# Optimization experiments

Measured on AMD Instinct MI355X. Metric: run time of the kernel, lower is better.

The kernel has to match this reference:

```python
import jax, jax.numpy as jnp
import numpy as np

EPS = 1e-5

def _layernorm(x, g, b):
    mu = jnp.mean(x, axis=-1, keepdims=True)
    var = jnp.var(x, axis=-1, keepdims=True)
    return (x - mu) * jax.lax.rsqrt(var + EPS) * g + b

def setup_inputs() -> dict:
    key = jax.random.key(0)
    ks = jax.random.split(key, 8)
    N, K, E, H = 20000, 32, 256, 128
    return {
        "edge_features": jax.random.normal(ks[0], (N, K, E), dtype=jnp.float32),
        "neighbor_mask": jax.random.randint(ks[1], (N, K), 0, 2) > 0,
        "W_lin": jax.random.normal(ks[2], (E, H), dtype=jnp.float32) / np.sqrt(E),
        "b_lin": jnp.zeros((H,), jnp.float32),
        "g_edge": jnp.ones((H,), jnp.float32),
        "b_edge": jnp.zeros((H,), jnp.float32),
        "W1": jax.random.normal(ks[3], (H, H), dtype=jnp.float32) / np.sqrt(H),
        "b1": jnp.zeros((H,), jnp.float32),
        "W2": jax.random.normal(ks[4], (H, H), dtype=jnp.float32) / np.sqrt(H),
        "b2": jnp.zeros((H,), jnp.float32),
        "g_node": jnp.ones((H,), jnp.float32),
        "b_node": jnp.zeros((H,), jnp.float32),
    }

def reference(edge_features, neighbor_mask, W_lin, b_lin, g_edge, b_edge,
              W1, b1, W2, b2, g_node, b_node):
    # edge_linear: [N,K,E] -> [N,K,H]
    edge_hidden = jnp.einsum('nke,eh->nkh', edge_features, W_lin) + b_lin
    # pre-norm FFN with residual: h + FFN(LN(h))
    h_norm = _layernorm(edge_hidden, g_edge, b_edge)
    ffn = jnp.einsum('nkh,hf->nkf', jax.nn.gelu(jnp.einsum('nkh,hf->nkf', h_norm, W1) + b1), W2) + b2
    edge_output = edge_hidden + ffn
    # masked scatter-aggregate over neighbors -> nodes
    mask = neighbor_mask[..., None].astype(edge_output.dtype)  # [N,K,1]
    node_output = jnp.sum(edge_output * mask, axis=1)  # [N,H]
    # block-level node normalization
    node_output = _layernorm(node_output, g_node, b_node)
    return (node_output, edge_output)
```

## Files before the change

### kernel.cpp

```cpp
#include <hip/hip_runtime.h>

typedef __attribute__((ext_vector_type(8))) short bfrag;
typedef __attribute__((ext_vector_type(4))) float ffrag;

struct alignas(16) U8v { unsigned int u[4]; };

__device__ __forceinline__ unsigned int cvt_pk_bf16(float lo, float hi) {
    unsigned int r;
    asm("v_cvt_pk_bf16_f32 %0, %1, %2" : "=v"(r) : "v"(lo), "v"(hi));
    return r;
}
__device__ __forceinline__ unsigned short f2bf1(float x) {
    return (unsigned short)cvt_pk_bf16(x, x);
}

__global__ void prep_kernel(const float* __restrict__ Wlin,
                            const float* __restrict__ W1,
                            const float* __restrict__ W2,
                            unsigned short* __restrict__ wlinT,
                            unsigned short* __restrict__ w1T,
                            unsigned short* __restrict__ w2T) {
    int idx = blockIdx.x * 256 + threadIdx.x;
    {
        int e = idx >> 7, h = idx & 127;
        wlinT[h * 256 + e] = f2bf1(Wlin[idx]);
    }
    if (idx < 128 * 128) {
        int h = idx >> 7, f = idx & 127;
        w1T[f * 128 + h] = f2bf1(W1[idx]);
        w2T[f * 128 + h] = f2bf1(W2[idx]);
    }
}

__global__ __launch_bounds__(512, 4) void fused_kernel(
    const float* __restrict__ ef, const int* __restrict__ mask,
    const unsigned short* __restrict__ wlinT,
    const unsigned short* __restrict__ w1T,
    const unsigned short* __restrict__ w2T,
    const float* __restrict__ b_lin, const float* __restrict__ g_edge,
    const float* __restrict__ b_edge, const float* __restrict__ b1,
    const float* __restrict__ b2, const float* __restrict__ g_node,
    const float* __restrict__ b_node,
    float* __restrict__ out_node, float* __restrict__ out_edge, int N) {

    __shared__ char  smem[32768];
    __shared__ float s_part[1024];
    __shared__ float s_stat[128];
    __shared__ float s_mask[64];
    __shared__ float s_nv[256];

    const int tid = threadIdx.x;
    const int w = tid >> 6, lane = tid & 63, q = lane >> 4, c = lane & 15;
    const int col = 16 * w + c;

    int row_base = blockIdx.x * 64;
    if (row_base + 64 > N * 32) row_base = N * 32 - 64;
    const int n0 = row_base >> 5;
    const float* efb = ef + (size_t)row_base * 256;

    if (tid < 64) s_mask[tid] = (mask[(size_t)row_base + tid] != 0) ? 1.f : 0.f;

    #pragma unroll
    for (int i = 0; i < 4; ++i) {
        int s = i * 512 + tid;
        int row = s >> 5, cs = s & 31;
        const float4* p = (const float4*)(efb + (size_t)s * 8);
        float4 v0 = p[0], v1 = p[1];
        U8v u;
        u.u[0] = cvt_pk_bf16(v0.x, v0.y); u.u[1] = cvt_pk_bf16(v0.z, v0.w);
        u.u[2] = cvt_pk_bf16(v1.x, v1.y); u.u[3] = cvt_pk_bf16(v1.z, v1.w);
        *(U8v*)(smem + row * 512 + ((cs * 16) ^ ((row & 7) << 4))) = u;
    }
    __syncthreads();

    ffrag acc[4] = {};
    #pragma unroll
    for (int kk = 0; kk < 8; ++kk) {
        bfrag b = *(const bfrag*)(wlinT + col * 256 + kk * 32 + q * 8);
        #pragma unroll
        for (int mt = 0; mt < 4; ++mt) {
            int row = 16 * mt + c;
            bfrag a = *(const bfrag*)(smem + row * 512 + ((kk * 64 + q * 16) ^ ((row & 7) << 4)));
            acc[mt] = __builtin_amdgcn_mfma_f32_16x16x32_bf16(a, b, acc[mt], 0, 0, 0);
        }
    }
    {
        float bl = b_lin[col];
        #pragma unroll
        for (int mt = 0; mt < 4; ++mt)
            #pragma unroll
            for (int r = 0; r < 4; ++r) acc[mt][r] += bl;
    }

    #pragma unroll
    for (int mt = 0; mt < 4; ++mt)
        #pragma unroll
        for (int r = 0; r < 4; ++r) {
            float s = acc[mt][r], qv = acc[mt][r] * acc[mt][r];
            #pragma unroll
            for (int d = 1; d < 16; d <<= 1) { s += __shfl_xor(s, d); qv += __shfl_xor(qv, d); }
            if (c == 0) {
                int row = 16 * mt + 4 * q + r;
                s_part[w * 128 + row * 2]     = s;
                s_part[w * 128 + row * 2 + 1] = qv;
            }
        }
    __syncthreads();
    if (tid < 64) {
        float s = 0.f, qv = 0.f;
        #pragma unroll
        for (int ww = 0; ww < 8; ++ww) { s += s_part[ww * 128 + tid * 2]; qv += s_part[ww * 128 + tid * 2 + 1]; }
        float mu = s * (1.f / 128.f);
        float var = qv * (1.f / 128.f) - mu * mu;
        s_stat[tid] = mu;
        s_stat[64 + tid] = rsqrtf(var + 1e-5f);
    }
    __syncthreads();

    {
        float ge = g_edge[col], be = b_edge[col];
        #pragma unroll
        for (int mt = 0; mt < 4; ++mt)
            #pragma unroll
            for (int r = 0; r < 4; ++r) {
                int row = 16 * mt + 4 * q + r;
                float x = (acc[mt][r] - s_stat[row]) * s_stat[64 + row] * ge + be;
                *(unsigned short*)(smem + row * 256 + ((col * 2) ^ ((row & 7) << 4))) = f2bf1(x);
            }
    }
    __syncthreads();

    ffrag acc2[4] = {};
    #pragma unroll
    for (int kk = 0; kk < 4; ++kk) {
        bfrag b = *(const bfrag*)(w1T + col * 128 + kk * 32 + q * 8);
        #pragma unroll
        for (int mt = 0; mt < 4; ++mt) {
            int row = 16 * mt + c;
            bfrag a = *(const bfrag*)(smem + row * 256 + ((kk * 64 + q * 16) ^ ((row & 7) << 4)));
            acc2[mt] = __builtin_amdgcn_mfma_f32_16x16x32_bf16(a, b, acc2[mt], 0, 0, 0);
        }
    }
    {
        float b1c = b1[col];
        #pragma unroll
        for (int mt = 0; mt < 4; ++mt)
            #pragma unroll
            for (int r = 0; r < 4; ++r) {
                int row = 16 * mt + 4 * q + r;
                float x = acc2[mt][r] + b1c;
                float y = 0.7978845608028654f * x * (1.f + 0.044715f * x * x);
                float e;
                asm("v_exp_f32 %0, %1" : "=v"(e) : "v"(-2.885390081777927f * y));
                float rcp;
                asm("v_rcp_f32 %0, %1" : "=v"(rcp) : "v"(1.f + e));
                float ge = x * rcp;
                *(unsigned short*)(smem + 16384 + row * 256 + ((col * 2) ^ ((row & 7) << 4))) = f2bf1(ge);
            }
    }
    __syncthreads();

    ffrag acc3[4] = {};
    #pragma unroll
    for (int kk = 0; kk < 4; ++kk) {
        bfrag b = *(const bfrag*)(w2T + col * 128 + kk * 32 + q * 8);
        #pragma unroll
        for (int mt = 0; mt < 4; ++mt) {
            int row = 16 * mt + c;
            bfrag a = *(const bfrag*)(smem + 16384 + row * 256 + ((kk * 64 + q * 16) ^ ((row & 7) << 4)));
            acc3[mt] = __builtin_amdgcn_mfma_f32_16x16x32_bf16(a, b, acc3[mt], 0, 0, 0);
        }
    }
    {
        float b2c = b2[col];
        float* eo = out_edge + (size_t)row_base * 128;
        float nvA = 0.f, nvB = 0.f;
        #pragma unroll
        for (int mt = 0; mt < 4; ++mt)
            #pragma unroll
            for (int r = 0; r < 4; ++r) {
                int row = 16 * mt + 4 * q + r;
                float v = acc3[mt][r] + b2c + acc[mt][r];
                eo[row * 128 + col] = v;
                float mv = s_mask[row] * v;
                if (mt < 2) nvA += mv; else nvB += mv;
            }
        nvA += __shfl_xor(nvA, 16); nvA += __shfl_xor(nvA, 32);
        nvB += __shfl_xor(nvB, 16); nvB += __shfl_xor(nvB, 32);
        if (q == 0) { s_nv[col] = nvA; s_nv[128 + col] = nvB; }
    }
    __syncthreads();

    if (w < 2) {
        float v0 = s_nv[w * 128 + lane], v1 = s_nv[w * 128 + 64 + lane];
        float s = v0 + v1, qv = v0 * v0 + v1 * v1;
        #pragma unroll
        for (int d = 1; d < 64; d <<= 1) { s += __shfl_xor(s, d); qv += __shfl_xor(qv, d); }
        float mu = s * (1.f / 128.f);
        float rstd = rsqrtf(qv * (1.f / 128.f) - mu * mu + 1e-5f);
        size_t base = (size_t)(n0 + w) * 128;
        out_node[base + lane]      = (v0 - mu) * rstd * g_node[lane]      + b_node[lane];
        out_node[base + 64 + lane] = (v1 - mu) * rstd * g_node[64 + lane] + b_node[64 + lane];
    }
}

extern "C" void kernel_launch(void* const* d_in, const int* in_sizes, int n_in,
                              void* d_out, int out_size, void* d_ws, size_t ws_size,
                              hipStream_t stream) {
    const float* ef     = (const float*)d_in[0];
    const int*   mask   = (const int*)d_in[1];
    const float* Wlin   = (const float*)d_in[2];
    const float* b_lin  = (const float*)d_in[3];
    const float* g_edge = (const float*)d_in[4];
    const float* b_edge = (const float*)d_in[5];
    const float* W1     = (const float*)d_in[6];
    const float* b1     = (const float*)d_in[7];
    const float* W2     = (const float*)d_in[8];
    const float* b2     = (const float*)d_in[9];
    const float* g_node = (const float*)d_in[10];
    const float* b_node = (const float*)d_in[11];

    int N = in_sizes[0] / (32 * 256);

    unsigned short* wlinT = (unsigned short*)d_ws;
    unsigned short* w1T   = wlinT + 128 * 256;
    unsigned short* w2T   = w1T + 128 * 128;

    float* out_node = (float*)d_out;
    float* out_edge = out_node + (size_t)N * 128;

    prep_kernel<<<128, 256, 0, stream>>>(Wlin, W1, W2, wlinT, w1T, w2T);
    int npairs = (N + 1) / 2;
    fused_kernel<<<npairs, 512, 0, stream>>>(ef, mask, wlinT, w1T, w2T,
                                             b_lin, g_edge, b_edge, b1, b2,
                                             g_node, b_node, out_node, out_edge, N);
}
```

Before: 356.5 us.

## Give each wave its own 16-row tile and fold LayerNorm affine into W1

The kernel now uses 256-thread blocks where each wave owns 16 edge rows across all 128 hidden columns. Edge features are loaded straight from global memory into MFMA fragments, so the shared staging step is gone, and LayerNorm statistics are reduced inside a wave with no block barriers. The edge-norm gain and bias are folded into a pre-scaled W1 and a fused bias by a new prep kernel. Edge outputs are staged through LDS for coalesced float4 stores. The intent is to remove most __syncthreads and LDS traffic, at the cost of more registers (8 accumulator tiles per stage) and weight fragments re-read from global memory per wave.

Result: slower. 715.2 us (+100.6%).

```diff
diff --git a/kernel.cpp b/kernel.cpp
--- a/kernel.cpp
+++ b/kernel.cpp
@@ -3,7 +3,7 @@
 typedef __attribute__((ext_vector_type(8))) short bfrag;
 typedef __attribute__((ext_vector_type(4))) float ffrag;
 
-struct alignas(16) U8v { unsigned int u[4]; };
+union BFU { bfrag f; unsigned int u[4]; };
 
 __device__ __forceinline__ unsigned int cvt_pk_bf16(float lo, float hi) {
     unsigned int r;
@@ -14,193 +14,174 @@
     return (unsigned short)cvt_pk_bf16(x, x);
 }
 
-__global__ void prep_kernel(const float* __restrict__ Wlin,
-                            const float* __restrict__ W1,
-                            const float* __restrict__ W2,
-                            unsigned short* __restrict__ wlinT,
-                            unsigned short* __restrict__ w1T,
-                            unsigned short* __restrict__ w2T) {
+__global__ void prep1(const float* __restrict__ Wlin, const float* __restrict__ W2,
+                      unsigned short* __restrict__ wlinT, unsigned short* __restrict__ w2T) {
     int idx = blockIdx.x * 256 + threadIdx.x;
-    {
-        int e = idx >> 7, h = idx & 127;
-        wlinT[h * 256 + e] = f2bf1(Wlin[idx]);
-    }
-    if (idx < 128 * 128) {
-        int h = idx >> 7, f = idx & 127;
-        w1T[f * 128 + h] = f2bf1(W1[idx]);
-        w2T[f * 128 + h] = f2bf1(W2[idx]);
-    }
-}
-
-__global__ __launch_bounds__(512, 4) void fused_kernel(
+    { int e = idx >> 7, h = idx & 127; wlinT[h * 256 + e] = f2bf1(Wlin[idx]); }
+    if (idx < 16384) { int a = idx >> 7, b = idx & 127; w2T[b * 128 + a] = f2bf1(W2[idx]); }
+}
+
+__global__ void prep2(const float* __restrict__ W1, const float* __restrict__ g_edge,
+                      const float* __restrict__ b_edge, const float* __restrict__ b1,
+                      unsigned short* __restrict__ w1gT, float* __restrict__ b1f) {
+    int f = threadIdx.x;
+    float s = b1[f];
+    for (int h = 0; h < 128; ++h) {
+        float wv = W1[h * 128 + f];
+        w1gT[f * 128 + h] = f2bf1(g_edge[h] * wv);
+        s += b_edge[h] * wv;
+    }
+    b1f[f] = s;
+}
+
+__global__ __launch_bounds__(256, 4) void fused_kernel(
     const float* __restrict__ ef, const int* __restrict__ mask,
     const unsigned short* __restrict__ wlinT,
-    const unsigned short* __restrict__ w1T,
+    const unsigned short* __restrict__ w1gT,
     const unsigned short* __restrict__ w2T,
-    const float* __restrict__ b_lin, const float* __restrict__ g_edge,
-    const float* __restrict__ b_edge, const float* __restrict__ b1,
+    const float* __restrict__ b_lin, const float* __restrict__ b1f,
     const float* __restrict__ b2, const float* __restrict__ g_node,
     const float* __restrict__ b_node,
     float* __restrict__ out_node, float* __restrict__ out_edge, int N) {
 
-    __shared__ char  smem[32768];
-    __shared__ float s_part[1024];
-    __shared__ float s_stat[128];
-    __shared__ float s_mask[64];
-    __shared__ float s_nv[256];
+    __shared__ char lds[4 * 8704];
+    __shared__ float nvlds[4][128];
 
     const int tid = threadIdx.x;
-    const int w = tid >> 6, lane = tid & 63, q = lane >> 4, c = lane & 15;
-    const int col = 16 * w + c;
-
-    int row_base = blockIdx.x * 64;
-    if (row_base + 64 > N * 32) row_base = N * 32 - 64;
-    const int n0 = row_base >> 5;
-    const float* efb = ef + (size_t)row_base * 256;
-
-    if (tid < 64) s_mask[tid] = (mask[(size_t)row_base + tid] != 0) ? 1.f : 0.f;
-
-    #pragma unroll
-    for (int i = 0; i < 4; ++i) {
-        int s = i * 512 + tid;
-        int row = s >> 5, cs = s & 31;
-        const float4* p = (const float4*)(efb + (size_t)s * 8);
-        float4 v0 = p[0], v1 = p[1];
-        U8v u;
-        u.u[0] = cvt_pk_bf16(v0.x, v0.y); u.u[1] = cvt_pk_bf16(v0.z, v0.w);
-        u.u[2] = cvt_pk_bf16(v1.x, v1.y); u.u[3] = cvt_pk_bf16(v1.z, v1.w);
-        *(U8v*)(smem + row * 512 + ((cs * 16) ^ ((row & 7) << 4))) = u;
+    const int w = tid >> 6, l = tid & 63, q = l >> 4, c = l & 15;
+
+    int rb_blk = blockIdx.x * 64;
+    if (rb_blk + 64 > N * 32) rb_blk = N * 32 - 64;
+    const int rb = rb_blk + w * 16;
+
+    char* Z  = lds + w * 8704;
+    char* G  = Z + 4352;
+    char* EO = Z;
+
+    ffrag h8[8] = {};
+    const float* efrow = ef + (size_t)(rb + c) * 256;
+    #pragma unroll 2
+    for (int kk = 0; kk < 8; ++kk) {
+        const float4* bp = (const float4*)(efrow + kk * 32 + 8 * q);
+        float4 e0 = bp[0], e1 = bp[1];
+        BFU bb;
+        bb.u[0] = cvt_pk_bf16(e0.x, e0.y); bb.u[1] = cvt_pk_bf16(e0.z, e0.w);
+        bb.u[2] = cvt_pk_bf16(e1.x, e1.y); bb.u[3] = cvt_pk_bf16(e1.z, e1.w);
+        #pragma unroll
+        for (int t = 0; t < 8; ++t) {
+            bfrag a = *(const bfrag*)(wlinT + (16 * t + c) * 256 + kk * 32 + 8 * q);
+            h8[t] = __builtin_amdgcn_mfma_f32_16x16x32_bf16(a, bb.f, h8[t], 0, 0, 0);
+        }
+    }
+
+    float sum = 0.f, sq = 0.f;
+    #pragma unroll
+    for (int t = 0; t < 8; ++t)
+        #pragma unroll
+        for (int r = 0; r < 4; ++r) {
+            float v = h8[t][r] + b_lin[16 * t + 4 * q + r];
+            h8[t][r] = v;
+            sum += v; sq += v * v;
+        }
+    sum += __shfl_xor(sum, 16); sum += __shfl_xor(sum, 32);
+    sq  += __shfl_xor(sq, 16);  sq  += __shfl_xor(sq, 32);
+    const float mu = sum * (1.f / 128.f);
+    const float rs = rsqrtf(sq * (1.f / 128.f) - mu * mu + 1e-5f);
+
+    #pragma unroll
+    for (int t = 0; t < 8; ++t) {
+        *(unsigned int*)(Z + c * 272 + 32 * t + 8 * q) =
+            cvt_pk_bf16((h8[t][0] - mu) * rs, (h8[t][1] - mu) * rs);
+        *(unsigned int*)(Z + c * 272 + 32 * t + 8 * q + 4) =
+            cvt_pk_bf16((h8[t][2] - mu) * rs, (h8[t][3] - mu) * rs);
+    }
+
+    ffrag acc2[8] = {};
+    #pragma unroll
+    for (int kk = 0; kk < 4; ++kk) {
+        bfrag zb = *(const bfrag*)(Z + c * 272 + kk * 64 + 16 * q);
+        #pragma unroll
+        for (int t = 0; t < 8; ++t) {
+            bfrag a = *(const bfrag*)(w1gT + (16 * t + c) * 128 + kk * 32 + 8 * q);
+            acc2[t] = __builtin_amdgcn_mfma_f32_16x16x32_bf16(a, zb, acc2[t], 0, 0, 0);
+        }
+    }
+
+    #pragma unroll
+    for (int t = 0; t < 8; ++t) {
+        float gg[4];
+        #pragma unroll
+        for (int r = 0; r < 4; ++r) {
+            float x = acc2[t][r] + b1f[16 * t + 4 * q + r];
+            float y = 0.7978845608028654f * x * (1.f + 0.044715f * x * x);
+            float e;
+            asm("v_exp_f32 %0, %1" : "=v"(e) : "v"(-2.885390081777927f * y));
+            float rcp;
+            asm("v_rcp_f32 %0, %1" : "=v"(rcp) : "v"(1.f + e));
+            gg[r] = x * rcp;
+        }
+        *(unsigned int*)(G + c * 272 + 32 * t + 8 * q)     = cvt_pk_bf16(gg[0], gg[1]);
+        *(unsigned int*)(G + c * 272 + 32 * t + 8 * q + 4) = cvt_pk_bf16(gg[2], gg[3]);
+    }
+
+    ffrag acc3[8] = {};
+    #pragma unroll
+    for (int kk = 0; kk < 4; ++kk) {
+        bfrag gb = *(const bfrag*)(G + c * 272 + kk * 64 + 16 * q);
+        #pragma unroll
+        for (int t = 0; t < 8; ++t) {
+            bfrag a = *(const bfrag*)(w2T + (16 * t + c) * 128 + kk * 32 + 8 * q);
+            acc3[t] = __builtin_amdgcn_mfma_f32_16x16x32_bf16(a, gb, acc3[t], 0, 0, 0);
+        }
+    }
+
+    #pragma unroll
+    for (int t = 0; t < 8; ++t)
+        #pragma unroll
+        for (int r = 0; r < 4; ++r) {
+            float v = acc3[t][r] + b2[16 * t + 4 * q + r] + h8[t][r];
+            *(float*)(EO + c * 528 + (16 * t + 4 * q + r) * 4) = v;
+        }
+
+    float4 nva = make_float4(0.f, 0.f, 0.f, 0.f);
+    float4 nvb = make_float4(0.f, 0.f, 0.f, 0.f);
+    float* eob = out_edge + (size_t)rb * 128;
+    #pragma unroll
+    for (int rr = 0; rr < 4; ++rr) {
+        int row = rr * 4 + q;
+        float4 va = *(const float4*)(EO + row * 528 + c * 16);
+        float4 vb = *(const float4*)(EO + row * 528 + 256 + c * 16);
+        *(float4*)(eob + row * 128 + c * 4)      = va;
+        *(float4*)(eob + row * 128 + 64 + c * 4) = vb;
+        float m = (mask[rb + row] != 0) ? 1.f : 0.f;
+        nva.x += m * va.x; nva.y += m * va.y; nva.z += m * va.z; nva.w += m * va.w;
+        nvb.x += m * vb.x; nvb.y += m * vb.y; nvb.z += m * vb.z; nvb.w += m * vb.w;
+    }
+    nva.x += __shfl_xor(nva.x, 16); nva.x += __shfl_xor(nva.x, 32);
+    nva.y += __shfl_xor(nva.y, 16); nva.y += __shfl_xor(nva.y, 32);
+    nva.z += __shfl_xor(nva.z, 16); nva.z += __shfl_xor(nva.z, 32);
+    nva.w += __shfl_xor(nva.w, 16); nva.w += __shfl_xor(nva.w, 32);
+    nvb.x += __shfl_xor(nvb.x, 16); nvb.x += __shfl_xor(nvb.x, 32);
+    nvb.y += __shfl_xor(nvb.y, 16); nvb.y += __shfl_xor(nvb.y, 32);
+    nvb.z += __shfl_xor(nvb.z, 16); nvb.z += __shfl_xor(nvb.z, 32);
+    nvb.w += __shfl_xor(nvb.w, 16); nvb.w += __shfl_xor(nvb.w, 32);
+    if (q == 0) {
+        *(float4*)(&nvlds[w][4 * c])      = nva;
+        *(float4*)(&nvlds[w][64 + 4 * c]) = nvb;
     }
     __syncthreads();
 
-    ffrag acc[4] = {};
-    #pragma unroll
-    for (int kk = 0; kk < 8; ++kk) {
-        bfrag b = *(const bfrag*)(wlinT + col * 256 + kk * 32 + q * 8);
-        #pragma unroll
-        for (int mt = 0; mt < 4; ++mt) {
-            int row = 16 * mt + c;
-            bfrag a = *(const bfrag*)(smem + row * 512 + ((kk * 64 + q * 16) ^ ((row & 7) << 4)));
-            acc[mt] = __builtin_amdgcn_mfma_f32_16x16x32_bf16(a, b, acc[mt], 0, 0, 0);
-        }
-    }
-    {
-        float bl = b_lin[col];
-        #pragma unroll
-        for (int mt = 0; mt < 4; ++mt)
-            #pragma unroll
-            for (int r = 0; r < 4; ++r) acc[mt][r] += bl;
-    }
-
-    #pragma unroll
-    for (int mt = 0; mt < 4; ++mt)
-        #pragma unroll
-        for (int r = 0; r < 4; ++r) {
-            float s = acc[mt][r], qv = acc[mt][r] * acc[mt][r];
-            #pragma unroll
-            for (int d = 1; d < 16; d <<= 1) { s += __shfl_xor(s, d); qv += __shfl_xor(qv, d); }
-            if (c == 0) {
-                int row = 16 * mt + 4 * q + r;
-                s_part[w * 128 + row * 2]     = s;
-                s_part[w * 128 + row * 2 + 1] = qv;
-            }
-        }
-    __syncthreads();
-    if (tid < 64) {
-        float s = 0.f, qv = 0.f;
-        #pragma unroll
-        for (int ww = 0; ww < 8; ++ww) { s += s_part[ww * 128 + tid * 2]; qv += s_part[ww * 128 + tid * 2 + 1]; }
-        float mu = s * (1.f / 128.f);
-        float var = qv * (1.f / 128.f) - mu * mu;
-        s_stat[tid] = mu;
-        s_stat[64 + tid] = rsqrtf(var + 1e-5f);
-    }
-    __syncthreads();
-
-    {
-        float ge = g_edge[col], be = b_edge[col];
-        #pragma unroll
-        for (int mt = 0; mt < 4; ++mt)
-            #pragma unroll
-            for (int r = 0; r < 4; ++r) {
-                int row = 16 * mt + 4 * q + r;
-                float x = (acc[mt][r] - s_stat[row]) * s_stat[64 + row] * ge + be;
-                *(unsigned short*)(smem + row * 256 + ((col * 2) ^ ((row & 7) << 4))) = f2bf1(x);
-            }
-    }
-    __syncthreads();
-
-    ffrag acc2[4] = {};
-    #pragma unroll
-    for (int kk = 0; kk < 4; ++kk) {
-        bfrag b = *(const bfrag*)(w1T + col * 128 + kk * 32 + q * 8);
-        #pragma unroll
-        for (int mt = 0; mt < 4; ++mt) {
-            int row = 16 * mt + c;
-            bfrag a = *(const bfrag*)(smem + row * 256 + ((kk * 64 + q * 16) ^ ((row & 7) << 4)));
-            acc2[mt] = __builtin_amdgcn_mfma_f32_16x16x32_bf16(a, b, acc2[mt], 0, 0, 0);
-        }
-    }
-    {
-        float b1c = b1[col];
-        #pragma unroll
-        for (int mt = 0; mt < 4; ++mt)
-            #pragma unroll
-            for (int r = 0; r < 4; ++r) {
-                int row = 16 * mt + 4 * q + r;
-                float x = acc2[mt][r] + b1c;
-                float y = 0.7978845608028654f * x * (1.f + 0.044715f * x * x);
-                float e;
-                asm("v_exp_f32 %0, %1" : "=v"(e) : "v"(-2.885390081777927f * y));
-                float rcp;
-                asm("v_rcp_f32 %0, %1" : "=v"(rcp) : "v"(1.f + e));
-                float ge = x * rcp;
-                *(unsigned short*)(smem + 16384 + row * 256 + ((col * 2) ^ ((row & 7) << 4))) = f2bf1(ge);
-            }
-    }
-    __syncthreads();
-
-    ffrag acc3[4] = {};
-    #pragma unroll
-    for (int kk = 0; kk < 4; ++kk) {
-        bfrag b = *(const bfrag*)(w2T + col * 128 + kk * 32 + q * 8);
-        #pragma unroll
-        for (int mt = 0; mt < 4; ++mt) {
-            int row = 16 * mt + c;
-            bfrag a = *(const bfrag*)(smem + 16384 + row * 256 + ((kk * 64 + q * 16) ^ ((row & 7) << 4)));
-            acc3[mt] = __builtin_amdgcn_mfma_f32_16x16x32_bf16(a, b, acc3[mt], 0, 0, 0);
-        }
-    }
-    {
-        float b2c = b2[col];
-        float* eo = out_edge + (size_t)row_base * 128;
-        float nvA = 0.f, nvB = 0.f;
-        #pragma unroll
-        for (int mt = 0; mt < 4; ++mt)
-            #pragma unroll
-            for (int r = 0; r < 4; ++r) {
-                int row = 16 * mt + 4 * q + r;
-                float v = acc3[mt][r] + b2c + acc[mt][r];
-                eo[row * 128 + col] = v;
-                float mv = s_mask[row] * v;
-                if (mt < 2) nvA += mv; else nvB += mv;
-            }
-        nvA += __shfl_xor(nvA, 16); nvA += __shfl_xor(nvA, 32);
-        nvB += __shfl_xor(nvB, 16); nvB += __shfl_xor(nvB, 32);
-        if (q == 0) { s_nv[col] = nvA; s_nv[128 + col] = nvB; }
-    }
-    __syncthreads();
-
     if (w < 2) {
-        float v0 = s_nv[w * 128 + lane], v1 = s_nv[w * 128 + 64 + lane];
+        float v0 = nvlds[2 * w][l]      + nvlds[2 * w + 1][l];
+        float v1 = nvlds[2 * w][64 + l] + nvlds[2 * w + 1][64 + l];
         float s = v0 + v1, qv = v0 * v0 + v1 * v1;
         #pragma unroll
         for (int d = 1; d < 64; d <<= 1) { s += __shfl_xor(s, d); qv += __shfl_xor(qv, d); }
-        float mu = s * (1.f / 128.f);
-        float rstd = rsqrtf(qv * (1.f / 128.f) - mu * mu + 1e-5f);
-        size_t base = (size_t)(n0 + w) * 128;
-        out_node[base + lane]      = (v0 - mu) * rstd * g_node[lane]      + b_node[lane];
-        out_node[base + 64 + lane] = (v1 - mu) * rstd * g_node[64 + lane] + b_node[64 + lane];
+        float mu2 = s * (1.f / 128.f);
+        float rstd = rsqrtf(qv * (1.f / 128.f) - mu2 * mu2 + 1e-5f);
+        size_t nb = ((size_t)(rb_blk >> 5) + w) * 128;
+        out_node[nb + l]      = (v0 - mu2) * rstd * g_node[l]      + b_node[l];
+        out_node[nb + 64 + l] = (v1 - mu2) * rstd * g_node[64 + l] + b_node[64 + l];
     }
 }
 
@@ -223,15 +204,17 @@
     int N = in_sizes[0] / (32 * 256);
 
     unsigned short* wlinT = (unsigned short*)d_ws;
-    unsigned short* w1T   = wlinT + 128 * 256;
-    unsigned short* w2T   = w1T + 128 * 128;
+    unsigned short* w1gT  = wlinT + 128 * 256;
+    unsigned short* w2T   = w1gT + 128 * 128;
+    float*          b1f   = (float*)(w2T + 128 * 128);
 
     float* out_node = (float*)d_out;
     float* out_edge = out_node + (size_t)N * 128;
 
-    prep_kernel<<<128, 256, 0, stream>>>(Wlin, W1, W2, wlinT, w1T, w2T);
-    int npairs = (N + 1) / 2;
-    fused_kernel<<<npairs, 512, 0, stream>>>(ef, mask, wlinT, w1T, w2T,
-                                             b_lin, g_edge, b_edge, b1, b2,
-                                             g_node, b_node, out_node, out_edge, N);
-}
+    prep1<<<128, 256, 0, stream>>>(Wlin, W2, wlinT, w2T);
+    prep2<<<1, 128, 0, stream>>>(W1, g_edge, b_edge, b1, w1gT, b1f);
+    int nblocks = (N * 32 + 63) / 64;
+    fused_kernel<<<nblocks, 256, 0, stream>>>(ef, mask, wlinT, w1gT, w2T,
+                                              b_lin, b1f, b2, g_node, b_node,
+                                              out_node, out_edge, N);
+}
```

## Process one node per block and feed edge features directly into MFMA registers

Applied to the files above, without the earlier changes.

Each block now handles one node (32 rows) instead of two, doubling the grid and raising launch_bounds occupancy to 8 blocks per CU. The first GEMM loads fp32 edge features straight from global memory into bf16 MFMA fragments, with no LDS staging and no barrier before it. Intermediate activations go into padded LDS arrays (stride 136) instead of XOR-swizzled buffers, and LDS use is reduced overall. The aim is more latency hiding through extra resident waves. The cost is that each block reuses the weight loads over half as many rows, and the global loads are now strided per lane rather than fully coalesced.

Result: slower. 868.8 us (+143.7%).

```diff
diff --git a/kernel.cpp b/kernel.cpp
--- a/kernel.cpp
+++ b/kernel.cpp
@@ -3,7 +3,7 @@
 typedef __attribute__((ext_vector_type(8))) short bfrag;
 typedef __attribute__((ext_vector_type(4))) float ffrag;
 
-struct alignas(16) U8v { unsigned int u[4]; };
+union BFU { bfrag f; unsigned int u[4]; };
 
 __device__ __forceinline__ unsigned int cvt_pk_bf16(float lo, float hi) {
     unsigned int r;
@@ -21,18 +21,15 @@
                             unsigned short* __restrict__ w1T,
                             unsigned short* __restrict__ w2T) {
     int idx = blockIdx.x * 256 + threadIdx.x;
-    {
-        int e = idx >> 7, h = idx & 127;
-        wlinT[h * 256 + e] = f2bf1(Wlin[idx]);
-    }
-    if (idx < 128 * 128) {
+    { int e = idx >> 7, h = idx & 127; wlinT[h * 256 + e] = f2bf1(Wlin[idx]); }
+    if (idx < 16384) {
         int h = idx >> 7, f = idx & 127;
         w1T[f * 128 + h] = f2bf1(W1[idx]);
         w2T[f * 128 + h] = f2bf1(W2[idx]);
     }
 }
 
-__global__ __launch_bounds__(512, 4) void fused_kernel(
+__global__ __launch_bounds__(512, 8) void fused_kernel(
     const float* __restrict__ ef, const int* __restrict__ mask,
     const unsigned short* __restrict__ wlinT,
     const unsigned short* __restrict__ w1T,
@@ -41,166 +38,149 @@
     const float* __restrict__ b_edge, const float* __restrict__ b1,
     const float* __restrict__ b2, const float* __restrict__ g_node,
     const float* __restrict__ b_node,
-    float* __restrict__ out_node, float* __restrict__ out_edge, int N) {
-
-    __shared__ char  smem[32768];
-    __shared__ float s_part[1024];
-    __shared__ float s_stat[128];
-    __shared__ float s_mask[64];
-    __shared__ float s_nv[256];
+    float* __restrict__ out_node, float* __restrict__ out_edge) {
+
+    __shared__ unsigned short s_hn[32 * 136];
+    __shared__ unsigned short s_g[32 * 136];
+    __shared__ float s_part[8 * 64];
+    __shared__ float s_stat[64];
+    __shared__ float s_mask[32];
+    __shared__ float s_nv[128];
 
     const int tid = threadIdx.x;
-    const int w = tid >> 6, lane = tid & 63, q = lane >> 4, c = lane & 15;
+    const int w = tid >> 6, l = tid & 63, q = l >> 4, c = l & 15;
     const int col = 16 * w + c;
-
-    int row_base = blockIdx.x * 64;
-    if (row_base + 64 > N * 32) row_base = N * 32 - 64;
-    const int n0 = row_base >> 5;
-    const float* efb = ef + (size_t)row_base * 256;
-
-    if (tid < 64) s_mask[tid] = (mask[(size_t)row_base + tid] != 0) ? 1.f : 0.f;
+    const int n = blockIdx.x;
+
+    if (tid < 32) s_mask[tid] = (mask[(size_t)n * 32 + tid] != 0) ? 1.f : 0.f;
+
+    ffrag h[2] = {};
+    const float* ef0 = ef + ((size_t)n * 32 + c) * 256;
+    const float* ef1 = ef0 + 16 * 256;
+    #pragma unroll 1
+    for (int kk = 0; kk < 8; ++kk) {
+        const float4* p0 = (const float4*)(ef0 + kk * 32 + 8 * q);
+        const float4* p1 = (const float4*)(ef1 + kk * 32 + 8 * q);
+        float4 a0 = p0[0], a1 = p0[1], b0 = p1[0], b1v = p1[1];
+        BFU fa, fb;
+        fa.u[0] = cvt_pk_bf16(a0.x, a0.y); fa.u[1] = cvt_pk_bf16(a0.z, a0.w);
+        fa.u[2] = cvt_pk_bf16(a1.x, a1.y); fa.u[3] = cvt_pk_bf16(a1.z, a1.w);
+        fb.u[0] = cvt_pk_bf16(b0.x, b0.y); fb.u[1] = cvt_pk_bf16(b0.z, b0.w);
+        fb.u[2] = cvt_pk_bf16(b1v.x, b1v.y); fb.u[3] = cvt_pk_bf16(b1v.z, b1v.w);
+        bfrag bw = *(const bfrag*)(wlinT + col * 256 + kk * 32 + 8 * q);
+        h[0] = __builtin_amdgcn_mfma_f32_16x16x32_bf16(fa.f, bw, h[0], 0, 0, 0);
+        h[1] = __builtin_amdgcn_mfma_f32_16x16x32_bf16(fb.f, bw, h[1], 0, 0, 0);
+    }
+    {
+        float blc = b_lin[col];
+        #pragma unroll
+        for (int m = 0; m < 2; ++m)
+            #pragma unroll
+            for (int r = 0; r < 4; ++r) h[m][r] += blc;
+    }
 
     #pragma unroll
-    for (int i = 0; i < 4; ++i) {
-        int s = i * 512 + tid;
-        int row = s >> 5, cs = s & 31;
-        const float4* p = (const float4*)(efb + (size_t)s * 8);
-        float4 v0 = p[0], v1 = p[1];
-        U8v u;
-        u.u[0] = cvt_pk_bf16(v0.x, v0.y); u.u[1] = cvt_pk_bf16(v0.z, v0.w);
-        u.u[2] = cvt_pk_bf16(v1.x, v1.y); u.u[3] = cvt_pk_bf16(v1.z, v1.w);
-        *(U8v*)(smem + row * 512 + ((cs * 16) ^ ((row & 7) << 4))) = u;
-    }
-    __syncthreads();
-
-    ffrag acc[4] = {};
-    #pragma unroll
-    for (int kk = 0; kk < 8; ++kk) {
-        bfrag b = *(const bfrag*)(wlinT + col * 256 + kk * 32 + q * 8);
-        #pragma unroll
-        for (int mt = 0; mt < 4; ++mt) {
-            int row = 16 * mt + c;
-            bfrag a = *(const bfrag*)(smem + row * 512 + ((kk * 64 + q * 16) ^ ((row & 7) << 4)));
-            acc[mt] = __builtin_amdgcn_mfma_f32_16x16x32_bf16(a, b, acc[mt], 0, 0, 0);
-        }
-    }
-    {
-        float bl = b_lin[col];
-        #pragma unroll
-        for (int mt = 0; mt < 4; ++mt)
-            #pragma unroll
-            for (int r = 0; r < 4; ++r) acc[mt][r] += bl;
-    }
-
-    #pragma unroll
-    for (int mt = 0; mt < 4; ++mt)
+    for (int m = 0; m < 2; ++m)
         #pragma unroll
         for (int r = 0; r < 4; ++r) {
-            float s = acc[mt][r], qv = acc[mt][r] * acc[mt][r];
+            float s = h[m][r], qv = h[m][r] * h[m][r];
             #pragma unroll
             for (int d = 1; d < 16; d <<= 1) { s += __shfl_xor(s, d); qv += __shfl_xor(qv, d); }
             if (c == 0) {
-                int row = 16 * mt + 4 * q + r;
-                s_part[w * 128 + row * 2]     = s;
-                s_part[w * 128 + row * 2 + 1] = qv;
+                int row = 16 * m + 4 * q + r;
+                s_part[w * 64 + row * 2]     = s;
+                s_part[w * 64 + row * 2 + 1] = qv;
             }
         }
     __syncthreads();
-    if (tid < 64) {
+    if (tid < 32) {
         float s = 0.f, qv = 0.f;
         #pragma unroll
-        for (int ww = 0; ww < 8; ++ww) { s += s_part[ww * 128 + tid * 2]; qv += s_part[ww * 128 + tid * 2 + 1]; }
+        for (int ww = 0; ww < 8; ++ww) { s += s_part[ww * 64 + tid * 2]; qv += s_part[ww * 64 + tid * 2 + 1]; }
         float mu = s * (1.f / 128.f);
-        float var = qv * (1.f / 128.f) - mu * mu;
         s_stat[tid] = mu;
-        s_stat[64 + tid] = rsqrtf(var + 1e-5f);
+        s_stat[32 + tid] = rsqrtf(qv * (1.f / 128.f) - mu * mu + 1e-5f);
     }
     __syncthreads();
 
     {
         float ge = g_edge[col], be = b_edge[col];
         #pragma unroll
-        for (int mt = 0; mt < 4; ++mt)
+        for (int m = 0; m < 2; ++m)
             #pragma unroll
             for (int r = 0; r < 4; ++r) {
-                int row = 16 * mt + 4 * q + r;
-                float x = (acc[mt][r] - s_stat[row]) * s_stat[64 + row] * ge + be;
-                *(unsigned short*)(smem + row * 256 + ((col * 2) ^ ((row & 7) << 4))) = f2bf1(x);
-            }
-    }
-    __syncthreads();
-
-    ffrag acc2[4] = {};
-    #pragma unroll
+                int row = 16 * m + 4 * q + r;
+                float x = (h[m][r] - s_stat[row]) * s_stat[32 + row] * ge + be;
+                s_hn[row * 136 + col] = f2bf1(x);
+            }
+    }
+    __syncthreads();
+
+    ffrag a2[2] = {};
+    #pragma unroll 2
     for (int kk = 0; kk < 4; ++kk) {
-        bfrag b = *(const bfrag*)(w1T + col * 128 + kk * 32 + q * 8);
-        #pragma unroll
-        for (int mt = 0; mt < 4; ++mt) {
-            int row = 16 * mt + c;
-            bfrag a = *(const bfrag*)(smem + row * 256 + ((kk * 64 + q * 16) ^ ((row & 7) << 4)));
-            acc2[mt] = __builtin_amdgcn_mfma_f32_16x16x32_bf16(a, b, acc2[mt], 0, 0, 0);
-        }
+        bfrag bw = *(const bfrag*)(w1T + col * 128 + kk * 32 + 8 * q);
+        bfrag x0 = *(const bfrag*)(s_hn + (c)      * 136 + kk * 32 + 8 * q);
+        bfrag x1 = *(const bfrag*)(s_hn + (16 + c) * 136 + kk * 32 + 8 * q);
+        a2[0] = __builtin_amdgcn_mfma_f32_16x16x32_bf16(x0, bw, a2[0], 0, 0, 0);
+        a2[1] = __builtin_amdgcn_mfma_f32_16x16x32_bf16(x1, bw, a2[1], 0, 0, 0);
     }
     {
         float b1c = b1[col];
         #pragma unroll
-        for (int mt = 0; mt < 4; ++mt)
+        for (int m = 0; m < 2; ++m)
             #pragma unroll
             for (int r = 0; r < 4; ++r) {
-                int row = 16 * mt + 4 * q + r;
-                float x = acc2[mt][r] + b1c;
+                int row = 16 * m + 4 * q + r;
+                float x = a2[m][r] + b1c;
                 float y = 0.7978845608028654f * x * (1.f + 0.044715f * x * x);
                 float e;
                 asm("v_exp_f32 %0, %1" : "=v"(e) : "v"(-2.885390081777927f * y));
                 float rcp;
                 asm("v_rcp_f32 %0, %1" : "=v"(rcp) : "v"(1.f + e));
-                float ge = x * rcp;
-                *(unsigned short*)(smem + 16384 + row * 256 + ((col * 2) ^ ((row & 7) << 4))) = f2bf1(ge);
-            }
-    }
-    __syncthreads();
-
-    ffrag acc3[4] = {};
-    #pragma unroll
+                s_g[row * 136 + col] = f2bf1(x * rcp);
+            }
+    }
+    __syncthreads();
+
+    ffrag a3[2] = {};
+    #pragma unroll 2
     for (int kk = 0; kk < 4; ++kk) {
-        bfrag b = *(const bfrag*)(w2T + col * 128 + kk * 32 + q * 8);
-        #pragma unroll
-        for (int mt = 0; mt < 4; ++mt) {
-            int row = 16 * mt + c;
-            bfrag a = *(const bfrag*)(smem + 16384 + row * 256 + ((kk * 64 + q * 16) ^ ((row & 7) << 4)));
-            acc3[mt] = __builtin_amdgcn_mfma_f32_16x16x32_bf16(a, b, acc3[mt], 0, 0, 0);
-        }
+        bfrag bw = *(const bfrag*)(w2T + col * 128 + kk * 32 + 8 * q);
+        bfrag x0 = *(const bfrag*)(s_g + (c)      * 136 + kk * 32 + 8 * q);
+        bfrag x1 = *(const bfrag*)(s_g + (16 + c) * 136 + kk * 32 + 8 * q);
+        a3[0] = __builtin_amdgcn_mfma_f32_16x16x32_bf16(x0, bw, a3[0], 0, 0, 0);
+        a3[1] = __builtin_amdgcn_mfma_f32_16x16x32_bf16(x1, bw, a3[1], 0, 0, 0);
     }
     {
         float b2c = b2[col];
-        float* eo = out_edge + (size_t)row_base * 128;
-        float nvA = 0.f, nvB = 0.f;
-        #pragma unroll
-        for (int mt = 0; mt < 4; ++mt)
+        float* eo = out_edge + (size_t)n * 4096;
+        float nv = 0.f;
+        #pragma unroll
+        for (int m = 0; m < 2; ++m)
             #pragma unroll
             for (int r = 0; r < 4; ++r) {
-                int row = 16 * mt + 4 * q + r;
-                float v = acc3[mt][r] + b2c + acc[mt][r];
+                int row = 16 * m + 4 * q + r;
+                float v = a3[m][r] + b2c + h[m][r];
                 eo[row * 128 + col] = v;
-                float mv = s_mask[row] * v;
-                if (mt < 2) nvA += mv; else nvB += mv;
-            }
-        nvA += __shfl_xor(nvA, 16); nvA += __shfl_xor(nvA, 32);
-        nvB += __shfl_xor(nvB, 16); nvB += __shfl_xor(nvB, 32);
-        if (q == 0) { s_nv[col] = nvA; s_nv[128 + col] = nvB; }
-    }
-    __syncthreads();
-
-    if (w < 2) {
-        float v0 = s_nv[w * 128 + lane], v1 = s_nv[w * 128 + 64 + lane];
+                nv += s_mask[row] * v;
+            }
+        nv += __shfl_xor(nv, 16);
+        nv += __shfl_xor(nv, 32);
+        if (q == 0) s_nv[col] = nv;
+    }
+    __syncthreads();
+
+    if (w == 0) {
+        float v0 = s_nv[l], v1 = s_nv[64 + l];
         float s = v0 + v1, qv = v0 * v0 + v1 * v1;
         #pragma unroll
         for (int d = 1; d < 64; d <<= 1) { s += __shfl_xor(s, d); qv += __shfl_xor(qv, d); }
-        float mu = s * (1.f / 128.f);
-        float rstd = rsqrtf(qv * (1.f / 128.f) - mu * mu + 1e-5f);
-        size_t base = (size_t)(n0 + w) * 128;
-        out_node[base + lane]      = (v0 - mu) * rstd * g_node[lane]      + b_node[lane];
-        out_node[base + 64 + lane] = (v1 - mu) * rstd * g_node[64 + lane] + b_node[64 + lane];
+        float mu2 = s * (1.f / 128.f);
+        float rstd = rsqrtf(qv * (1.f / 128.f) - mu2 * mu2 + 1e-5f);
+        size_t nb = (size_t)n * 128;
+        out_node[nb + l]      = (v0 - mu2) * rstd * g_node[l]      + b_node[l];
+        out_node[nb + 64 + l] = (v1 - mu2) * rstd * g_node[64 + l] + b_node[64 + l];
     }
 }
 
@@ -230,8 +210,7 @@
     float* out_edge = out_node + (size_t)N * 128;
 
     prep_kernel<<<128, 256, 0, stream>>>(Wlin, W1, W2, wlinT, w1T, w2T);
-    int npairs = (N + 1) / 2;
-    fused_kernel<<<npairs, 512, 0, stream>>>(ef, mask, wlinT, w1T, w2T,
-                                             b_lin, g_edge, b_edge, b1, b2,
-                                             g_node, b_node, out_node, out_edge, N);
-}
+    fused_kernel<<<N, 512, 0, stream>>>(ef, mask, wlinT, w1T, w2T,
+                                        b_lin, g_edge, b_edge, b1, b2,
+                                        g_node, b_node, out_node, out_edge);
+}
```

## Process four nodes per block with padded LDS layout for FFN stages

Applied to the files above, without the earlier changes.

Each block now handles 128 edge rows (four nodes) instead of 64, doubling the M tiles per wave so each loaded weight fragment feeds twice as many MFMAs. LDS grows to about 68 KB and the intermediate activations use a padded 136-element row stride in place of the XOR swizzle. The per-block reduction and node layernorm are widened to four nodes. The larger LDS footprint and doubled accumulator registers likely lower occupancy, and the boundary clamp for odd N was dropped, so N must be a multiple of four.

Result: faster. 305.2 us (-14.4%).

```diff
diff --git a/kernel.cpp b/kernel.cpp
--- a/kernel.cpp
+++ b/kernel.cpp
@@ -21,11 +21,8 @@
                             unsigned short* __restrict__ w1T,
                             unsigned short* __restrict__ w2T) {
     int idx = blockIdx.x * 256 + threadIdx.x;
-    {
-        int e = idx >> 7, h = idx & 127;
-        wlinT[h * 256 + e] = f2bf1(Wlin[idx]);
-    }
-    if (idx < 128 * 128) {
+    { int e = idx >> 7, h = idx & 127; wlinT[h * 256 + e] = f2bf1(Wlin[idx]); }
+    if (idx < 16384) {
         int h = idx >> 7, f = idx & 127;
         w1T[f * 128 + h] = f2bf1(W1[idx]);
         w2T[f * 128 + h] = f2bf1(W2[idx]);
@@ -41,27 +38,27 @@
     const float* __restrict__ b_edge, const float* __restrict__ b1,
     const float* __restrict__ b2, const float* __restrict__ g_node,
     const float* __restrict__ b_node,
-    float* __restrict__ out_node, float* __restrict__ out_edge, int N) {
-
-    __shared__ char  smem[32768];
-    __shared__ float s_part[1024];
-    __shared__ float s_stat[128];
-    __shared__ float s_mask[64];
-    __shared__ float s_nv[256];
+    float* __restrict__ out_node, float* __restrict__ out_edge) {
+
+    __shared__ char  smem[69632];
+    __shared__ float s_stat[256];
+    __shared__ float s_mask[128];
+    __shared__ float s_nv[4 * 128];
+
+    float* s_part = (float*)smem;
+    unsigned short* s_hn = (unsigned short*)smem;
+    unsigned short* s_g  = (unsigned short*)(smem + 34816);
 
     const int tid = threadIdx.x;
-    const int w = tid >> 6, lane = tid & 63, q = lane >> 4, c = lane & 15;
+    const int w = tid >> 6, l = tid & 63, q = l >> 4, c = l & 15;
     const int col = 16 * w + c;
-
-    int row_base = blockIdx.x * 64;
-    if (row_base + 64 > N * 32) row_base = N * 32 - 64;
-    const int n0 = row_base >> 5;
-    const float* efb = ef + (size_t)row_base * 256;
-
-    if (tid < 64) s_mask[tid] = (mask[(size_t)row_base + tid] != 0) ? 1.f : 0.f;
+    const int rb = blockIdx.x * 128;
+    const float* efb = ef + (size_t)rb * 256;
+
+    if (tid < 128) s_mask[tid] = (mask[(size_t)rb + tid] != 0) ? 1.f : 0.f;
 
     #pragma unroll
-    for (int i = 0; i < 4; ++i) {
+    for (int i = 0; i < 8; ++i) {
         int s = i * 512 + tid;
         int row = s >> 5, cs = s & 31;
         const float4* p = (const float4*)(efb + (size_t)s * 8);
@@ -73,134 +70,141 @@
     }
     __syncthreads();
 
-    ffrag acc[4] = {};
+    ffrag h[8] = {};
     #pragma unroll
     for (int kk = 0; kk < 8; ++kk) {
-        bfrag b = *(const bfrag*)(wlinT + col * 256 + kk * 32 + q * 8);
-        #pragma unroll
-        for (int mt = 0; mt < 4; ++mt) {
+        bfrag bw = *(const bfrag*)(wlinT + col * 256 + kk * 32 + 8 * q);
+        #pragma unroll
+        for (int mt = 0; mt < 8; ++mt) {
             int row = 16 * mt + c;
             bfrag a = *(const bfrag*)(smem + row * 512 + ((kk * 64 + q * 16) ^ ((row & 7) << 4)));
-            acc[mt] = __builtin_amdgcn_mfma_f32_16x16x32_bf16(a, b, acc[mt], 0, 0, 0);
-        }
-    }
-    {
-        float bl = b_lin[col];
-        #pragma unroll
-        for (int mt = 0; mt < 4; ++mt)
-            #pragma unroll
-            for (int r = 0; r < 4; ++r) acc[mt][r] += bl;
-    }
+            h[mt] = __builtin_amdgcn_mfma_f32_16x16x32_bf16(a, bw, h[mt], 0, 0, 0);
+        }
+    }
+    {
+        float blc = b_lin[col];
+        #pragma unroll
+        for (int mt = 0; mt < 8; ++mt)
+            #pragma unroll
+            for (int r = 0; r < 4; ++r) h[mt][r] += blc;
+    }
+    __syncthreads();
 
     #pragma unroll
-    for (int mt = 0; mt < 4; ++mt)
+    for (int mt = 0; mt < 8; ++mt)
         #pragma unroll
         for (int r = 0; r < 4; ++r) {
-            float s = acc[mt][r], qv = acc[mt][r] * acc[mt][r];
+            float s = h[mt][r], qv = h[mt][r] * h[mt][r];
             #pragma unroll
             for (int d = 1; d < 16; d <<= 1) { s += __shfl_xor(s, d); qv += __shfl_xor(qv, d); }
             if (c == 0) {
                 int row = 16 * mt + 4 * q + r;
-                s_part[w * 128 + row * 2]     = s;
-                s_part[w * 128 + row * 2 + 1] = qv;
-            }
-        }
-    __syncthreads();
-    if (tid < 64) {
+                s_part[w * 256 + row * 2]     = s;
+                s_part[w * 256 + row * 2 + 1] = qv;
+            }
+        }
+    __syncthreads();
+    if (tid < 128) {
         float s = 0.f, qv = 0.f;
         #pragma unroll
-        for (int ww = 0; ww < 8; ++ww) { s += s_part[ww * 128 + tid * 2]; qv += s_part[ww * 128 + tid * 2 + 1]; }
+        for (int ww = 0; ww < 8; ++ww) { s += s_part[ww * 256 + tid * 2]; qv += s_part[ww * 256 + tid * 2 + 1]; }
         float mu = s * (1.f / 128.f);
-        float var = qv * (1.f / 128.f) - mu * mu;
         s_stat[tid] = mu;
-        s_stat[64 + tid] = rsqrtf(var + 1e-5f);
+        s_stat[128 + tid] = rsqrtf(qv * (1.f / 128.f) - mu * mu + 1e-5f);
     }
     __syncthreads();
 
     {
         float ge = g_edge[col], be = b_edge[col];
         #pragma unroll
-        for (int mt = 0; mt < 4; ++mt)
+        for (int mt = 0; mt < 8; ++mt)
             #pragma unroll
             for (int r = 0; r < 4; ++r) {
                 int row = 16 * mt + 4 * q + r;
-                float x = (acc[mt][r] - s_stat[row]) * s_stat[64 + row] * ge + be;
-                *(unsigned short*)(smem + row * 256 + ((col * 2) ^ ((row & 7) << 4))) = f2bf1(x);
-            }
-    }
-    __syncthreads();
-
-    ffrag acc2[4] = {};
-    #pragma unroll
-    for (int kk = 0; kk < 4; ++kk) {
-        bfrag b = *(const bfrag*)(w1T + col * 128 + kk * 32 + q * 8);
-        #pragma unroll
-        for (int mt = 0; mt < 4; ++mt) {
-            int row = 16 * mt + c;
-            bfrag a = *(const bfrag*)(smem + row * 256 + ((kk * 64 + q * 16) ^ ((row & 7) << 4)));
-            acc2[mt] = __builtin_amdgcn_mfma_f32_16x16x32_bf16(a, b, acc2[mt], 0, 0, 0);
-        }
-    }
-    {
+                float x = (h[mt][r] - s_stat[row]) * s_stat[128 + row] * ge + be;
+                s_hn[row * 136 + col] = f2bf1(x);
+            }
+    }
+    __syncthreads();
+
+    {
+        ffrag a2[8] = {};
+        #pragma unroll
+        for (int kk = 0; kk < 4; ++kk) {
+            bfrag bw = *(const bfrag*)(w1T + col * 128 + kk * 32 + 8 * q);
+            #pragma unroll
+            for (int mt = 0; mt < 8; ++mt) {
+                bfrag x = *(const bfrag*)(s_hn + (16 * mt + c) * 136 + kk * 32 + 8 * q);
+                a2[mt] = __builtin_amdgcn_mfma_f32_16x16x32_bf16(x, bw, a2[mt], 0, 0, 0);
+            }
+        }
         float b1c = b1[col];
         #pragma unroll
-        for (int mt = 0; mt < 4; ++mt)
+        for (int mt = 0; mt < 8; ++mt)
             #pragma unroll
             for (int r = 0; r < 4; ++r) {
                 int row = 16 * mt + 4 * q + r;
-                float x = acc2[mt][r] + b1c;
+                float x = a2[mt][r] + b1c;
                 float y = 0.7978845608028654f * x * (1.f + 0.044715f * x * x);
                 float e;
                 asm("v_exp_f32 %0, %1" : "=v"(e) : "v"(-2.885390081777927f * y));
                 float rcp;
                 asm("v_rcp_f32 %0, %1" : "=v"(rcp) : "v"(1.f + e));
-                float ge = x * rcp;
-                *(unsigned short*)(smem + 16384 + row * 256 + ((col * 2) ^ ((row & 7) << 4))) = f2bf1(ge);
-            }
-    }
-    __syncthreads();
-
-    ffrag acc3[4] = {};
-    #pragma unroll
-    for (int kk = 0; kk < 4; ++kk) {
-        bfrag b = *(const bfrag*)(w2T + col * 128 + kk * 32 + q * 8);
-        #pragma unroll
-        for (int mt = 0; mt < 4; ++mt) {
-            int row = 16 * mt + c;
-            bfrag a = *(const bfrag*)(smem + 16384 + row * 256 + ((kk * 64 + q * 16) ^ ((row & 7) << 4)));
-            acc3[mt] = __builtin_amdgcn_mfma_f32_16x16x32_bf16(a, b, acc3[mt], 0, 0, 0);
-        }
-    }
-    {
+                s_g[row * 136 + col] = f2bf1(x * rcp);
+            }
+    }
+    __syncthreads();
+
+    {
+        ffrag a3[8] = {};
+        #pragma unroll
+        for (int kk = 0; kk < 4; ++kk) {
+            bfrag bw = *(const bfrag*)(w2T + col * 128 + kk * 32 + 8 * q);
+            #pragma unroll
+            for (int mt = 0; mt < 8; ++mt) {
+                bfrag x = *(const bfrag*)(s_g + (16 * mt + c) * 136 + kk * 32 + 8 * q);
+                a3[mt] = __builtin_amdgcn_mfma_f32_16x16x32_bf16(x, bw, a3[mt], 0, 0, 0);
+            }
+        }
         float b2c = b2[col];
-        float* eo = out_edge + (size_t)row_base * 128;
-        float nvA = 0.f, nvB = 0.f;
-        #pragma unroll
-        for (int mt = 0; mt < 4; ++mt)
+        float* eo = out_edge + (size_t)rb * 128;
+        float nv0 = 0.f, nv1 = 0.f, nv2 = 0.f, nv3 = 0.f;
+        #pragma unroll
+        for (int mt = 0; mt < 8; ++mt)
             #pragma unroll
             for (int r = 0; r < 4; ++r) {
                 int row = 16 * mt + 4 * q + r;
-                float v = acc3[mt][r] + b2c + acc[mt][r];
+                float v = a3[mt][r] + b2c + h[mt][r];
                 eo[row * 128 + col] = v;
                 float mv = s_mask[row] * v;
-                if (mt < 2) nvA += mv; else nvB += mv;
-            }
-        nvA += __shfl_xor(nvA, 16); nvA += __shfl_xor(nvA, 32);
-        nvB += __shfl_xor(nvB, 16); nvB += __shfl_xor(nvB, 32);
-        if (q == 0) { s_nv[col] = nvA; s_nv[128 + col] = nvB; }
-    }
-    __syncthreads();
-
-    if (w < 2) {
-        float v0 = s_nv[w * 128 + lane], v1 = s_nv[w * 128 + 64 + lane];
+                if (mt < 2)      nv0 += mv;
+                else if (mt < 4) nv1 += mv;
+                else if (mt < 6) nv2 += mv;
+                else             nv3 += mv;
+            }
+        nv0 += __shfl_xor(nv0, 16); nv0 += __shfl_xor(nv0, 32);
+        nv1 += __shfl_xor(nv1, 16); nv1 += __shfl_xor(nv1, 32);
+        nv2 += __shfl_xor(nv2, 16); nv2 += __shfl_xor(nv2, 32);
+        nv3 += __shfl_xor(nv3, 16); nv3 += __shfl_xor(nv3, 32);
+        if (q == 0) {
+            s_nv[col]       = nv0;
+            s_nv[128 + col] = nv1;
+            s_nv[256 + col] = nv2;
+            s_nv[384 + col] = nv3;
+        }
+    }
+    __syncthreads();
+
+    if (w < 4) {
+        float v0 = s_nv[w * 128 + l], v1 = s_nv[w * 128 + 64 + l];
         float s = v0 + v1, qv = v0 * v0 + v1 * v1;
         #pragma unroll
         for (int d = 1; d < 64; d <<= 1) { s += __shfl_xor(s, d); qv += __shfl_xor(qv, d); }
-        float mu = s * (1.f / 128.f);
-        float rstd = rsqrtf(qv * (1.f / 128.f) - mu * mu + 1e-5f);
-        size_t base = (size_t)(n0 + w) * 128;
-        out_node[base + lane]      = (v0 - mu) * rstd * g_node[lane]      + b_node[lane];
-        out_node[base + 64 + lane] = (v1 - mu) * rstd * g_node[64 + lane] + b_node[64 + lane];
+        float mu2 = s * (1.f / 128.f);
+        float rstd = rsqrtf(qv * (1.f / 128.f) - mu2 * mu2 + 1e-5f);
+        size_t nb = ((size_t)(rb >> 5) + w) * 128;
+        out_node[nb + l]      = (v0 - mu2) * rstd * g_node[l]      + b_node[l];
+        out_node[nb + 64 + l] = (v1 - mu2) * rstd * g_node[64 + l] + b_node[64 + l];
     }
 }
 
@@ -230,8 +234,8 @@
     float* out_edge = out_node + (size_t)N * 128;
 
     prep_kernel<<<128, 256, 0, stream>>>(Wlin, W1, W2, wlinT, w1T, w2T);
-    int npairs = (N + 1) / 2;
-    fused_kernel<<<npairs, 512, 0, stream>>>(ef, mask, wlinT, w1T, w2T,
-                                             b_lin, g_edge, b_edge, b1, b2,
-                                             g_node, b_node, out_node, out_edge, N);
-}
+    int nblocks = (N * 32 + 127) / 128;
+    fused_kernel<<<nblocks, 512, 0, stream>>>(ef, mask, wlinT, w1T, w2T,
+                                              b_lin, g_edge, b_edge, b1, b2,
+                                              g_node, b_node, out_node, out_edge);
+}
```
